# Kernel optimization log

Hardware: AMD Instinct MI355X
Metric: run time of the kernel (lower is better)

Reference implementation:

```python
import jax, jax.numpy as jnp
import numpy as np

B, C, H, W = 2, 256, 56, 56
NH = 8
HD = C // NH
SCALE = HD ** -0.5
BN_EPS = 1e-5


def _linear(x, w, b=None):
    y = jnp.einsum('...i,oi->...o', x, w)
    return y + b if b is not None else y


def _dwconv3(v, w, b):
    # depthwise 3x3, stride 1, pad 1
    y = jax.lax.conv_general_dilated(v, w, (1, 1), 'SAME',
                                     dimension_numbers=('NCHW', 'OIHW', 'NCHW'),
                                     feature_group_count=C)
    return y + b[None, :, None, None]


def _spectral(x, context, qw, kvw, pw, pb, dww, dwb):
    # SpectralCrossAttention, sr_ratio=1 path
    xt = jnp.transpose(x, (0, 2, 3, 1))                    # B,H,W,C
    q = jnp.transpose(_linear(xt, qw), (0, 3, 1, 2))       # B,C,H,W
    ct = jnp.transpose(context, (0, 2, 3, 1))
    kv = _linear(ct, kvw)                                  # B,H,W,2C -> split [2,C]
    k = jnp.transpose(kv[..., :C], (0, 3, 1, 2))
    v = jnp.transpose(kv[..., C:], (0, 3, 1, 2))
    v_local = _dwconv3(v, dww, dwb)
    qf = jnp.fft.rfft2(q, s=(H, W), axes=(-2, -1), norm='ortho')
    kf = jnp.fft.rfft2(k, s=(H, W), axes=(-2, -1), norm='ortho')
    attn_map = jnp.fft.irfft2(qf * kf, s=(H, W), axes=(-2, -1), norm='ortho')
    out = attn_map * v + v_local
    out = _linear(jnp.transpose(out, (0, 2, 3, 1)), pw, pb)
    return jnp.transpose(out, (0, 3, 1, 2))


def _token(x, context, qw, kvw, pw, pb, cw):
    # TokenSpectralResidualCrossAttention, sr_ratio=1 path (de_conv = Identity)
    N = H * W
    xt = jnp.transpose(x.reshape(B, C, N), (0, 2, 1))       # B,N,C
    ct = jnp.transpose(context.reshape(B, C, N), (0, 2, 1))
    q = jnp.transpose(_linear(xt, qw).reshape(B, N, NH, HD), (0, 2, 1, 3))  # B,NH,N,HD
    kv = _linear(ct, kvw).reshape(B, N, 2, NH, HD)
    k = jnp.transpose(kv[:, :, 0], (0, 2, 1, 3))
    v = jnp.transpose(kv[:, :, 1], (0, 2, 1, 3))            # B,NH,N,HD
    attn = jax.nn.softmax(jnp.einsum('bhnd,bhmd->bhnm', q, k) * SCALE, axis=-1)
    x_attn = jnp.transpose(jnp.einsum('bhnm,bhmd->bhnd', attn, v), (0, 2, 1, 3)).reshape(B, N, C)
    v_img = jnp.transpose(v, (0, 1, 3, 2)).reshape(B, C, H, W)
    vf = jnp.fft.rfft2(v_img, s=(H, W), axes=(-2, -1), norm='ortho')
    weight = cw[..., 0] + 1j * cw[..., 1]                   # C,H,W//2+1 complex
    v_res = jnp.fft.irfft2(vf * weight[None], s=(H, W), axes=(-2, -1), norm='ortho')
    v_res = jnp.transpose(v_res.reshape(B, C, N), (0, 2, 1))
    out = _linear(x_attn + v_res, pw, pb)
    return jnp.transpose(out, (0, 2, 1)).reshape(B, C, H, W)


def _fuse(os_, ot, g_w1, g_bn_g, g_bn_b, g_w2, g_b2):
    # spatial_gate: Conv1x1(2C->C, no bias) -> BN(eval: mean0/var1) -> ReLU -> Conv1x1(C->1) -> Sigmoid
    g_in = jnp.concatenate([os_, ot], axis=1)               # B,2C,H,W
    h = jnp.einsum('oc,bchw->bohw', g_w1, g_in)
    h = h / jnp.sqrt(1.0 + BN_EPS) * g_bn_g[None, :, None, None] + g_bn_b[None, :, None, None]
    h = jax.nn.relu(h)
    gate = jax.nn.sigmoid(jnp.einsum('oc,bchw->bohw', g_w2, h) + g_b2[None, :, None, None])
    return gate * os_ + (1.0 - gate) * ot


def setup_inputs():
    key = jax.random.key(0)
    ks = jax.random.split(key, 14)
    p = lambda i, shape, s=0.02: jax.random.normal(ks[i], shape, jnp.float32) * s
    return {
        'x': jax.random.normal(ks[0], (B, C, H, W), jnp.float32),
        'context': jax.random.normal(ks[1], (B, C, H, W), jnp.float32),
        's_q_w': p(2, (C, C)),
        's_kv_w': p(3, (2 * C, C)),
        's_proj_w': p(4, (C, C)),
        's_proj_b': jnp.zeros((C,), jnp.float32),
        's_dw_w': p(5, (C, 1, 3, 3), float(np.sqrt(2.0 / 9.0))),
        's_dw_b': jnp.zeros((C,), jnp.float32),
        't_q_w': p(6, (C, C)),
        't_kv_w': p(7, (2 * C, C)),
        't_proj_w': p(8, (C, C)),
        't_proj_b': jnp.zeros((C,), jnp.float32),
        't_cw': p(9, (C, H, W // 2 + 1, 2)),
        'g_w1': p(10, (C, 2 * C), float(np.sqrt(2.0 / C))),
        'g_bn_g': jnp.ones((C,), jnp.float32),
        'g_bn_b': jnp.zeros((C,), jnp.float32),
        'g_w2': p(11, (1, C), float(np.sqrt(2.0 / C))),
        'g_b2': jnp.zeros((1,), jnp.float32),
    }


def reference(x, context, s_q_w, s_kv_w, s_proj_w, s_proj_b, s_dw_w, s_dw_b,
              t_q_w, t_kv_w, t_proj_w, t_proj_b, t_cw,
              g_w1, g_bn_g, g_bn_b, g_w2, g_b2):
    os_ = _spectral(x, context, s_q_w, s_kv_w, s_proj_w, s_proj_b, s_dw_w, s_dw_b)
    ot = _token(x, context, t_q_w, t_kv_w, t_proj_w, t_proj_b, t_cw)
    return _fuse(os_, ot, g_w1, g_bn_g, g_bn_b, g_w2, g_b2)
```

## Files before the change

### kernel.cpp

```cpp
#include <hip/hip_runtime.h>

namespace {
constexpr int kB = 2;
constexpr int kC = 256;
constexpr int kH = 56;
constexpr int kW = 56;
constexpr int kN = kH * kW;
constexpr int kNH = 8;
constexpr int kHD = 32;
constexpr int kNF = kW / 2 + 1;
constexpr int kSpec = kH * kNF;
constexpr long kCN = (long)kC * kN;
constexpr float kAttScale = 0.17677669529663687f;
constexpr float kLog2e = 1.4426950408889634f;
constexpr float kAng = 6.283185307179586f / 56.0f;
constexpr int TW1F = 0;
constexpr int TW2F = 8192;
constexpr int TW1I = 12288;
constexpr int TW2I = 20480;
constexpr int TWTOT = 24576;
}

typedef __attribute__((ext_vector_type(8))) short short8;
typedef __attribute__((ext_vector_type(4))) float float4v;
// ... 11 lines not shown
}
__device__ __forceinline__ float b2f(unsigned short u) {
    return __uint_as_float((unsigned)u << 16);
}
__device__ __forceinline__ unsigned f2b_pk(float a, float b) {
    unsigned ua = __float_as_uint(a); ua = (ua + 0x7FFFu + ((ua >> 16) & 1u)) >> 16;
    unsigned ub = __float_as_uint(b); ub = (ub + 0x7FFFu + ((ub >> 16) & 1u)) >> 16;
    return ua | (ub << 16);
}
__device__ __forceinline__ unsigned pk_trunc(float a, float b) {
    return (__float_as_uint(a) >> 16) | (__float_as_uint(b) & 0xFFFF0000u);
}
__device__ __forceinline__ uint4 pk8(const float* v) {
    return make_uint4(f2b_pk(v[0], v[1]), f2b_pk(v[2], v[3]),
                      f2b_pk(v[4], v[5]), f2b_pk(v[6], v[7]));
}

__device__ void twiddle_body(int blk, unsigned short* __restrict__ tw)
{
    int idx = blk * 256 + threadIdx.x;
    if (idx >= TWTOT) return;
    float val = 0.f;
    if (idx < TW2F) {
        int r = idx >> 6, c = idx & 63;
        if (c < 56) {
            if (r < 56)       val = cosf(kAng * (float)((r * c) % 56));
            else if (r < 112) val = sinf(kAng * (float)(((r - 56) * c) % 56));
        }
    } else if (idx < TW1I) {
        int t = idx - TW2F; int r = t >> 6, c = t & 63;
        if (c < 56) {
            if (r < 29)                  val = cosf(kAng * (float)((r * c) % 56));
            else if (r >= 32 && r < 61)  val = sinf(kAng * (float)(((r - 32) * c) % 56));
        }
    } else if (idx < TW2I) {
        int t = idx - TW1I; int r = t >> 6, c = t & 63;
        if (c < 56) {
            if (r < 56)                  val = cosf(kAng * (float)((r * c) % 56));
            else if (r >= 64 && r < 120) val = sinf(kAng * (float)(((r - 64) * c) % 56));
        }
    } else {
        int t = idx - TW2I; int x = t >> 6, c = t & 63;
        if (x < 56 && c < 58) {
            int v = c >> 1;
            float wv = ((v == 0) || (v == 28)) ? 1.f : 2.f;
            float a = kAng * (float)((v * x) % 56);
            val = (c & 1) ? (-wv * sinf(a)) : (wv * cosf(a));
        }
    }
    tw[idx] = f2b(val);
}

__device__ void gemm_bias_body(char* smem, const float* __restrict__ Wm,
                               const float* __restrict__ Xb,
                               const float* __restrict__ bias, float* __restrict__ Yb,
                               int o0, int oY, int n0, int CI)
{
    unsigned short (*Wt)[40] = (unsigned short(*)[40])smem;
    unsigned short (*Xt)[40] = (unsigned short(*)[40])(smem + 5120);

    const int tid = threadIdx.x;
    const int wave = tid >> 6, lane = tid & 63;
    const int ln = lane & 15, qd = lane >> 4;
    const int wy = wave >> 1, wx = wave & 1;

    const int ow = tid >> 2, kcw = tid & 3;
    const int nx = tid & 127, kcx = tid >> 7;
    const bool xvalid = (n0 + nx) < kN;

    float4v acc[2][4];
#pragma unroll
    for (int i = 0; i < 2; ++i)
#pragma unroll
        for (int j = 0; j < 4; ++j) acc[i][j] = (float4v){0.f, 0.f, 0.f, 0.f};

    float wpre[8], xpre[16];
    {
        const float* ws = Wm + (long)(o0 + ow) * CI + kcw * 8;
        *(float4*)&wpre[0] = *(const float4*)ws;
        *(float4*)&wpre[4] = *(const float4*)(ws + 4);
#pragma unroll
        for (int j = 0; j < 16; ++j)
            xpre[j] = xvalid ? Xb[(long)(kcx * 16 + j) * kN + n0 + nx] : 0.f;
    }

    for (int k0 = 0; k0 < CI; k0 += 32) {
        *(uint4*)&Wt[ow][kcw * 8]      = pk8(wpre);
        *(uint4*)&Xt[nx][kcx * 16]     = pk8(xpre);
        *(uint4*)&Xt[nx][kcx * 16 + 8] = pk8(xpre + 8);
        __syncthreads();

        if (k0 + 32 < CI) {
            const float* ws = Wm + (long)(o0 + ow) * CI + k0 + 32 + kcw * 8;
            *(float4*)&wpre[0] = *(const float4*)ws;
            *(float4*)&wpre[4] = *(const float4*)(ws + 4);
#pragma unroll
            for (int j = 0; j < 16; ++j)
                xpre[j] = xvalid ? Xb[(long)(k0 + 32 + kcx * 16 + j) * kN + n0 + nx] : 0.f;
        }

        Frag af[2], bf4[4];
#pragma unroll
        for (int mt = 0; mt < 2; ++mt)
            af[mt].u4 = *(const uint4*)&Wt[wy * 32 + mt * 16 + ln][qd * 8];
#pragma unroll
        for (int nt = 0; nt < 4; ++nt)
            bf4[nt].u4 = *(const uint4*)&Xt[wx * 64 + nt * 16 + ln][qd * 8];
#pragma unroll
        for (int mt = 0; mt < 2; ++mt)
#pragma unroll
            for (int nt = 0; nt < 4; ++nt)
                acc[mt][nt] = __builtin_amdgcn_mfma_f32_16x16x32_bf16(
                    af[mt].s, bf4[nt].s, acc[mt][nt], 0, 0, 0);
        __syncthreads();
    }

#pragma unroll
    for (int mt = 0; mt < 2; ++mt) {
        const int obL = o0 + wy * 32 + mt * 16 + qd * 4;
        const int obY = oY + wy * 32 + mt * 16 + qd * 4;
#pragma unroll
        for (int nt = 0; nt < 4; ++nt) {
            const int n = n0 + wx * 64 + nt * 16 + ln;
            if (n < kN) {
#pragma unroll
                for (int r = 0; r < 4; ++r) {
                    float v = acc[mt][nt][r];
                    if (bias) v += bias[obL + r];
                    Yb[(long)(obY + r) * kN + n] = v;
                }
            }
        }
    }
}

__global__ __launch_bounds__(256)
void init_proj_kernel(unsigned short* __restrict__ tw,
                      const float* __restrict__ x, const float* __restrict__ ctx,
                      const float* __restrict__ s_q_w, const float* __restrict__ t_q_w,
                      const float* __restrict__ s_kv_w, const float* __restrict__ t_kv_w,
                      float* __restrict__ sq, float* __restrict__ tq,
                      float* __restrict__ skv, float* __restrict__ tkv)
{
    __shared__ __align__(16) char smem[15360];
    int bi = blockIdx.x;
    if (bi < 96) { twiddle_body(bi, tw); return; }
    bi -= 96;
    if (bi < 400) {
        int b = bi / 200, rem = bi % 200;
        int y = rem / 25, xb = rem % 25;
        int sel = y >= 4;
        int o0 = (sel ? y - 4 : y) * 64;
        gemm_bias_body(smem, sel ? t_q_w : s_q_w, (x + (long)b * kCN), nullptr,
                       (sel ? tq : sq) + (long)b * kCN, o0, o0, xb * 128, kC);
    } else {
        bi -= 400;
        int b = bi / 400, rem = bi % 400;
        int y = rem / 25, xb = rem % 25;
        int sel = y >= 8;
        int o0 = (sel ? y - 8 : y) * 64;
        gemm_bias_body(smem, sel ? t_kv_w : s_kv_w, (ctx + (long)b * kCN), nullptr,
                       (sel ? tkv : skv) + (long)b * 2 * kCN, o0, o0, xb * 128, kC);
    }
}

__device__ void dft_fwd_body(char* smem, int bx,
                             const float* __restrict__ s0, const float* __restrict__ s1,
                             const float* __restrict__ s2, float* __restrict__ d0,
                             float* __restrict__ d1, float* __restrict__ d2,
                             const unsigned short* __restrict__ tw)
{
    const int which = bx >> 9, ch = bx & 511;
    const int b = ch >> 8, c = ch & 255;
    const float* src; long stride; float* spec;
    if (which == 0)      { src = s0; stride = kCN;     spec = d0; }
    else if (which == 1) { src = s1; stride = 2 * kCN; spec = d1; }
    else                 { src = s2; stride = 2 * kCN; spec = d2; }
    const float* img = src + (long)b * stride + (long)c * kN;

    unsigned short (*Gb)[72]    = (unsigned short(*)[72])smem;
    unsigned short (*imgT)[72]  = (unsigned short(*)[72])(smem + 18432);
    unsigned short (*Yb)[116]   = (unsigned short(*)[116])(smem + 18432);

    const int tid = threadIdx.x;
    const int wave = tid >> 6, lane = tid & 63;
    const int ln = lane & 15, qd = lane >> 4;

    for (int i = tid; i < 64 * 72; i += 256) {
        int r = i / 72, cc = i - r * 72;
        if (r >= 56 || cc >= 56) imgT[r][cc] = 0;
    }
    for (int i = tid; i < kN; i += 256) {
        int y = i / 56, x = i - y * 56;
        imgT[x][y] = f2b(img[i]);
    }
    __syncthreads();

    float4v acc1[2][4];
#pragma unroll
    for (int m = 0; m < 2; ++m)
#pragma unroll
        for (int n = 0; n < 4; ++n) acc1[m][n] = (float4v){0.f, 0.f, 0.f, 0.f};
#pragma unroll
    for (int ks = 0; ks < 2; ++ks) {
        Frag a[2], bf[4];
#pragma unroll
        for (int m = 0; m < 2; ++m)
            a[m].u4 = *(const uint4*)(tw + TW1F + ((2 * wave + m) * 16 + ln) * 64 + ks * 32 + qd * 8);
#pragma unroll
        for (int n = 0; n < 4; ++n)
            bf[n].u4 = *(const uint4*)&imgT[n * 16 + ln][ks * 32 + qd * 8];
#pragma unroll
        for (int m = 0; m < 2; ++m)
#pragma unroll
            for (int n = 0; n < 4; ++n)
                acc1[m][n] = __builtin_amdgcn_mfma_f32_16x16x32_bf16(a[m].s, bf[n].s, acc1[m][n], 0, 0, 0);
    }
#pragma unroll
    for (int m = 0; m < 2; ++m)
#pragma unroll
        for (int n = 0; n < 4; ++n)
#pragma unroll
            for (int r = 0; r < 4; ++r)
                Gb[(2 * wave + m) * 16 + qd * 4 + r][n * 16 + ln] = f2b(acc1[m][n][r]);
    __syncthreads();

    float4v acc2[7];
#pragma unroll
    for (int n = 0; n < 7; ++n) acc2[n] = (float4v){0.f, 0.f, 0.f, 0.f};
#pragma unroll
    for (int ks = 0; ks < 2; ++ks) {
        Frag a;
        a.u4 = *(const uint4*)(tw + TW2F + (wave * 16 + ln) * 64 + ks * 32 + qd * 8);
#pragma unroll
        for (int n = 0; n < 7; ++n) {
            Frag bb;
            bb.u4 = *(const uint4*)&Gb[n * 16 + ln][ks * 32 + qd * 8];
            acc2[n] = __builtin_amdgcn_mfma_f32_16x16x32_bf16(a.s, bb.s, acc2[n], 0, 0, 0);
        }
    }
#pragma unroll
    for (int n = 0; n < 7; ++n)
#pragma unroll
        for (int r = 0; r < 4; ++r)
            Yb[wave * 16 + qd * 4 + r][n * 16 + ln] = f2b(acc2[n][r]);
    __syncthreads();

    float2* outp = (float2*)spec + (long)ch * kSpec;
    for (int i = tid; i < kSpec; i += 256) {
        int u = i / kNF, v = i - u * kNF;
        float Qr = b2f(Yb[v][u]) - b2f(Yb[32 + v][56 + u]);
        float Qi = -b2f(Yb[32 + v][u]) - b2f(Yb[v][56 + u]);
        outp[i] = make_float2(Qr, Qi);
    }
}

__device__ void prepack_body(char* smem, int blk, const float* __restrict__ tkv,
                             unsigned short* __restrict__ Kp,
                             unsigned short* __restrict__ Vp)
{
    const int i = blk % 49;
    const int h = (blk / 49) & 7;
    const int b = blk / (49 * 8);
    const float* kb = tkv + (long)b * 2 * kCN + (long)h * kHD * kN;
    const float* vb = kb + kCN;
    const int tid = threadIdx.x;

    float (*Ks)[72] = (float(*)[72])smem;
#pragma unroll
    for (int j = 0; j < 8; ++j) {
        int e = tid + j * 256;
        int d = e >> 6, c = e & 63;
        Ks[d][c] = kb[(long)d * kN + i * 64 + c];
    }
    __syncthreads();
    {
        int tl = tid >> 6, lnn = (tid >> 2) & 15, qdd = tid & 3;
        float v[8];
#pragma unroll
        for (int j = 0; j < 8; ++j) v[j] = Ks[qdd * 8 + j][tl * 16 + lnn];
        unsigned short* dst = Kp + ((long)(b * 8 + h) * 196 + 4 * i + tl) * 512 + lnn * 32 + qdd * 8;
        *(uint4*)dst = pk8(v);
    }
    {
        int g = tid >> 7, dh = (tid >> 6) & 1, lnn = (tid >> 2) & 15, qdd = tid & 3;
        int d = dh * 16 + lnn;
        const float* src = vb + (long)d * kN + i * 64 + g * 32 + qdd * 8;
        float v[8];
        *(float4*)&v[0] = *(const float4*)src;
        *(float4*)&v[4] = *(const float4*)(src + 4);
        unsigned short* dst = Vp + ((long)(b * 8 + h) * 49 + i) * 2048 + ((g * 2 + dh) * 16 + lnn) * 32 + qdd * 8;
        *(uint4*)dst = pk8(v);
    }
}

__global__ __launch_bounds__(256)
void fwd3_prepack_kernel(const float* __restrict__ s0, const float* __restrict__ s1,
                         const float* __restrict__ s2, float* __restrict__ d0,
                         float* __restrict__ d1, float* __restrict__ d2,
                         const unsigned short* __restrict__ tw,
                         const float* __restrict__ tkv,
                         unsigned short* __restrict__ Kp, unsigned short* __restrict__ Vp)
{
    __shared__ __align__(16) char smem[33280];
    if (blockIdx.x < 1536)
        dft_fwd_body(smem, blockIdx.x, s0, s1, s2, d0, d1, d2, tw);
    else
        prepack_body(smem, blockIdx.x - 1536, tkv, Kp, Vp);
}

__device__ void dft_inv_body(char* smem, int bx,
                             const float* __restrict__ fQ, const float* __restrict__ fK,
                             const float* __restrict__ fV, const float* __restrict__ cw,
                             float* __restrict__ dst1, float* __restrict__ dst2,
                             const float* __restrict__ skvp, const float* __restrict__ dww,
                             const float* __restrict__ dwb, const unsigned short* __restrict__ tw)
{
    const int unit = bx >> 9;
    const int ch = bx & 511;
    const int b = ch >> 8, c = ch & 255;
    unsigned short (*Pb)[72]  = (unsigned short(*)[72])smem;
    unsigned short (*Yb)[72]  = (unsigned short(*)[72])(smem + 9216);
    unsigned short (*T2)[72]  = (unsigned short(*)[72])smem;
    float (*svs)[65]          = (float(*)[65])(smem + 9216);

    const int tid = threadIdx.x;
    const int wave = tid >> 6, lane = tid & 63;
    const int ln = lane & 15, qd = lane >> 4;

    const float2* Pin; const float2* Min; float scale; float* dst;
    if (unit == 0) {
        Pin = (const float2*)fQ + (long)ch * kSpec;
        Min = (const float2*)fK + (long)ch * kSpec;
        scale = 1.0f / 175616.0f; dst = dst1;
    } else {
        Pin = (const float2*)fV + (long)ch * kSpec;
        Min = (const float2*)cw + (long)c * kSpec;
        scale = 1.0f / 3136.0f; dst = dst2;
    }

    for (int i = tid; i < 64 * 72; i += 256) {
        int r = i / 72, cc = i - r * 72;
        if (r >= 58 || cc >= 56) Pb[r][cc] = 0;
    }
    for (int i = tid; i < kSpec; i += 256) {
        int u = i / kNF, v = i - u * kNF;
        float2 p = Pin[i];
        float2 m = Min[i];
        float pr = (p.x * m.x - p.y * m.y) * scale;
        float pi = (p.x * m.y + p.y * m.x) * scale;
        Pb[2 * v][u]     = f2b(pr);
        Pb[2 * v + 1][u] = f2b(pi);
    }
    __syncthreads();

    float4v acc1[2][4];
#pragma unroll
    for (int m = 0; m < 2; ++m)
#pragma unroll
        for (int n = 0; n < 4; ++n) acc1[m][n] = (float4v){0.f, 0.f, 0.f, 0.f};
#pragma unroll
// ... 47 lines not shown
        }
#pragma unroll
        for (int j = 0; j < 9; ++j) wreg[j] = dww[c * 9 + j];
        bias = dwb[c];
    }

    float4v acc2[4];
#pragma unroll
    for (int n = 0; n < 4; ++n) acc2[n] = (float4v){0.f, 0.f, 0.f, 0.f};
#pragma unroll
    for (int ks = 0; ks < 2; ++ks) {
        Frag a;
        a.u4 = *(const uint4*)(tw + TW2I + (wave * 16 + ln) * 64 + ks * 32 + qd * 8);
#pragma unroll
        for (int n = 0; n < 4; ++n) {
            Frag bb;
            bb.u4 = *(const uint4*)&T2[n * 16 + ln][ks * 32 + qd * 8];
            acc2[n] = __builtin_amdgcn_mfma_f32_16x16x32_bf16(a.s, bb.s, acc2[n], 0, 0, 0);
        }
    }
    __syncthreads();

    float* outd = dst + (long)ch * kN;
#pragma unroll
    for (int n = 0; n < 4; ++n) {
        int y = n * 16 + ln;
        if (y < 56) {
#pragma unroll
            for (int r = 0; r < 4; ++r) {
                int x = wave * 16 + qd * 4 + r;
                if (x < 56) {
                    int e = y * 56 + x;
                    if (unit == 0) {
                        float s = bias;
                        s = fmaf(wreg[0], svs[y][x],     s);
                        s = fmaf(wreg[1], svs[y][x + 1], s);
                        s = fmaf(wreg[2], svs[y][x + 2], s);
                        s = fmaf(wreg[3], svs[y + 1][x],     s);
                        s = fmaf(wreg[4], svs[y + 1][x + 1], s);
                        s = fmaf(wreg[5], svs[y + 1][x + 2], s);
                        s = fmaf(wreg[6], svs[y + 2][x],     s);
                        s = fmaf(wreg[7], svs[y + 2][x + 1], s);
                        s = fmaf(wreg[8], svs[y + 2][x + 2], s);
                        outd[e] = fmaf(acc2[n][r], svs[y + 1][x + 1], s);
                    } else {
                        outd[e] = acc2[n][r];
                    }
                }
            }
        }
    }
}

__device__ void attn_body(char* smem, int abi,
                          const float* __restrict__ tq,
                          const unsigned short* __restrict__ Kp,
                          const unsigned short* __restrict__ Vp,
                          float* __restrict__ Op, float* __restrict__ lp)
{
    const int xcd = abi & 7;
    const int t = abi >> 3;
    const int gsel = (t >= 100) ? 1 : 0;
    const int r0 = t - gsel * 100;
    const int grpId = (gsel << 3) | xcd;
    const int b = grpId >> 3, h = grpId & 7;
    const int sp = r0 / 25;
    const int q0 = (r0 % 25) * 128;
    const int tid = threadIdx.x;
    const int wave = tid >> 6, lane = tid & 63;
    const int qd = lane >> 4, ln = lane & 15;
    const int i0 = (sp == 0) ? 0 : (12 * sp + 1);
    const int i1 = 12 * sp + 13;

    const float* qb = tq + (long)b * kCN + (long)h * kHD * kN;
    const unsigned short* KpB = Kp + (long)(b * 8 + h) * 196 * 512 + ln * 32 + qd * 8;
    const unsigned short* VpB = Vp + (long)(b * 8 + h) * 49 * 2048 + ln * 32 + qd * 8;

    unsigned short* PsW = (unsigned short*)smem + wave * (32 * 40);

    const float qscale = kAttScale * kLog2e;
    Frag qf[2];
#pragma unroll
    for (int qt = 0; qt < 2; ++qt) {
        int qg = q0 + wave * 32 + qt * 16 + ln;
        bool qv = qg < kN;
#pragma unroll
        for (int j = 0; j < 8; ++j) {
            int d = qd * 8 + j;
            float v = qv ? qb[(long)d * kN + qg] * qscale : 0.f;
            qf[qt].u[j] = f2b(v);
        }
    }

    float4v o[2][2];
#pragma unroll
    for (int qt = 0; qt < 2; ++qt)
#pragma unroll
        for (int dh = 0; dh < 2; ++dh) o[qt][dh] = (float4v){0.f, 0.f, 0.f, 0.f};
    float lsum[2] = {0.f, 0.f};

    unsigned W[4][2][2];
    Frag ka[4];
#pragma unroll
    for (int m = 0; m < 4; ++m)
        ka[m].u4 = *(const uint4*)(KpB + (long)(4 * i0 + m) * 512);

    auto computeW = [&]() {
#pragma unroll
        for (int m = 0; m < 4; ++m) {
            float4v s0 = __builtin_amdgcn_mfma_f32_16x16x32_bf16(
                ka[m].s, qf[0].s, (float4v){0.f, 0.f, 0.f, 0.f}, 0, 0, 0);
            float4v s1 = __builtin_amdgcn_mfma_f32_16x16x32_bf16(
                ka[m].s, qf[1].s, (float4v){0.f, 0.f, 0.f, 0.f}, 0, 0, 0);
            float a0 = __builtin_amdgcn_exp2f(s0[0]);
            float a1 = __builtin_amdgcn_exp2f(s0[1]);
            float a2 = __builtin_amdgcn_exp2f(s0[2]);
            float a3 = __builtin_amdgcn_exp2f(s0[3]);
            lsum[0] += (a0 + a1) + (a2 + a3);
            W[m][0][0] = pk_trunc(a0, a1);
            W[m][0][1] = pk_trunc(a2, a3);
            float b0 = __builtin_amdgcn_exp2f(s1[0]);
            float b1 = __builtin_amdgcn_exp2f(s1[1]);
            float b2 = __builtin_amdgcn_exp2f(s1[2]);
            float b3 = __builtin_amdgcn_exp2f(s1[3]);
            lsum[1] += (b0 + b1) + (b2 + b3);
            W[m][1][0] = pk_trunc(b0, b1);
            W[m][1][1] = pk_trunc(b2, b3);
        }
    };

    computeW();
    if (i0 + 1 < i1) {
#pragma unroll
        for (int m = 0; m < 4; ++m)
            ka[m].u4 = *(const uint4*)(KpB + (long)(4 * (i0 + 1) + m) * 512);
    }

    for (int i = i0; i < i1; ++i) {
        Frag va[2][2];
#pragma unroll
        for (int g = 0; g < 2; ++g)
#pragma unroll
            for (int dh = 0; dh < 2; ++dh)
                va[g][dh].u4 = *(const uint4*)(VpB + (long)i * 2048 + (g * 2 + dh) * 512);

#pragma unroll
        for (int m = 0; m < 4; ++m)
#pragma unroll
            for (int qt = 0; qt < 2; ++qt)
                *(uint2*)&PsW[(qt * 16 + ln) * 40 + m * 16 + qd * 4] =
                    make_uint2(W[m][qt][0], W[m][qt][1]);

        if (i + 1 < i1) {
            computeW();
            if (i + 2 < i1) {
#pragma unroll
                for (int m = 0; m < 4; ++m)
                    ka[m].u4 = *(const uint4*)(KpB + (long)(4 * (i + 2) + m) * 512);
            }
        }

#pragma unroll
        for (int g = 0; g < 2; ++g) {
            Frag pa[2];
#pragma unroll
            for (int qt = 0; qt < 2; ++qt)
                pa[qt].u4 = *(const uint4*)&PsW[(qt * 16 + ln) * 40 + g * 32 + qd * 8];
#pragma unroll
            for (int qt = 0; qt < 2; ++qt)
#pragma unroll
                for (int dh = 0; dh < 2; ++dh)
                    o[qt][dh] = __builtin_amdgcn_mfma_f32_16x16x32_bf16(
                        pa[qt].s, va[g][dh].s, o[qt][dh], 0, 0, 0);
        }
    }

    const long grp = (long)(sp * 16 + b * 8 + h);
#pragma unroll
    for (int qt = 0; qt < 2; ++qt) {
        lsum[qt] += __shfl_xor(lsum[qt], 16, 64);
        lsum[qt] += __shfl_xor(lsum[qt], 32, 64);
        if (qd == 0)
            lp[grp * 3200 + q0 + wave * 32 + qt * 16 + ln] = lsum[qt];
#pragma unroll
        for (int dh = 0; dh < 2; ++dh)
#pragma unroll
            for (int r = 0; r < 4; ++r) {
                int q = q0 + wave * 32 + qt * 16 + qd * 4 + r;
                Op[(grp * 3200 + q) * 32 + dh * 16 + ln] = o[qt][dh][r];
            }
    }
}

__global__ __launch_bounds__(256, 4)
void inv_attn_kernel(const float* __restrict__ fQ, const float* __restrict__ fK,
                     const float* __restrict__ fV, const float* __restrict__ cw,
                     float* __restrict__ dst1, float* __restrict__ dst2,
                     const float* __restrict__ skvp, const float* __restrict__ dww,
                     const float* __restrict__ dwb, const unsigned short* __restrict__ tw,
                     const float* __restrict__ tq,
                     const unsigned short* __restrict__ Kp,
                     const unsigned short* __restrict__ Vp,
                     float* __restrict__ Op, float* __restrict__ lp)
{
    __shared__ __align__(16) char smem[27648];
    const int per = blockIdx.x / 328;
    const int off = blockIdx.x % 328;
    if (off < 128)
        dft_inv_body(smem, per * 128 + off, fQ, fK, fV, cw, dst1, dst2, skvp, dww, dwb, tw);
    else
        attn_body(smem, per * 200 + (off - 128), tq, Kp, Vp, Op, lp);
}

__global__ __launch_bounds__(256)
void attn_combine_kernel(const float* __restrict__ Op, const float* __restrict__ lp,
                         float* __restrict__ xo)
{
    const int qc = blockIdx.x, bh = blockIdx.y;
    const int b = bh >> 3, h = bh & 7;
    const int q0 = qc * 64;
    __shared__ float T[32][65];
    const int tid = threadIdx.x;

    for (int i = tid; i < 64 * 32; i += 256) {
        int ql = i >> 5, d = i & 31;
        float ov = 0.f, l = 0.f;
#pragma unroll
        for (int s = 0; s < 4; ++s) {
            long g = (long)(s * 16 + bh);
            ov += Op[(g * 3200 + q0 + ql) * 32 + d];
            l  += lp[g * 3200 + q0 + ql];
        }
        T[d][ql] = ov / l;
    }
    __syncthreads();
    for (int i = tid; i < 32 * 64; i += 256) {
        int d = i >> 6, ql = i & 63;
        xo[(long)b * kCN + (long)(h * kHD + d) * kN + q0 + ql] += T[d][ql];
    }
}

__global__ __launch_bounds__(256)
void gemm_fused(const float* __restrict__ W0, const float* __restrict__ W1,
                const float* __restrict__ X0, const float* __restrict__ X1,
                const float* __restrict__ b0, const float* __restrict__ b1,
                float* __restrict__ Y0, float* __restrict__ Y1,
                int oHalf, int CI, long xbs, long ybs, int oOffset)
{
    __shared__ __align__(16) char smem[15360];
    const int b  = blockIdx.z;
    const int sel = blockIdx.y >= oHalf;
    const int o0 = (sel ? blockIdx.y - oHalf : blockIdx.y) * 64;
    const int oY = o0 + (sel ? oOffset : 0);
    gemm_bias_body(smem, sel ? W1 : W0, (sel ? X1 : X0) + (long)b * xbs,
                   sel ? b1 : b0, (sel ? Y1 : Y0) + (long)b * ybs,
                   o0, oY, blockIdx.x * 128, CI);
}

__global__ __launch_bounds__(256)
void gemm_bn_kernel(const float* __restrict__ Wm, const float* __restrict__ X,
                    const float* __restrict__ gamma, const float* __restrict__ beta,
                    float* __restrict__ Y, int CI, long xbs, long ybs)
{
    const int b  = blockIdx.z;
    const int o0 = blockIdx.y * 64;
    const int n0 = blockIdx.x * 128;
    const float* Xb = X + (long)b * xbs;
    float* Yb = Y + (long)b * ybs;

    __shared__ __align__(16) unsigned short Wt[64][40];
    __shared__ __align__(16) unsigned short Xt[128][40];

    const int tid = threadIdx.x;
    const int wave = tid >> 6, lane = tid & 63;
    const int ln = lane & 15, qd = lane >> 4;
    const int wy = wave >> 1, wx = wave & 1;

    const int ow = tid >> 2, kcw = tid & 3;
    const int nx = tid & 127, kcx = tid >> 7;
    const bool xvalid = (n0 + nx) < kN;

    float4v acc[2][4];
#pragma unroll
    for (int i = 0; i < 2; ++i)
#pragma unroll
        for (int j = 0; j < 4; ++j) acc[i][j] = (float4v){0.f, 0.f, 0.f, 0.f};

    float wpre[8], xpre[16];
    {
        const float* ws = Wm + (long)(o0 + ow) * CI + kcw * 8;
        *(float4*)&wpre[0] = *(const float4*)ws;
        *(float4*)&wpre[4] = *(const float4*)(ws + 4);
#pragma unroll
        for (int j = 0; j < 16; ++j)
            xpre[j] = xvalid ? Xb[(long)(kcx * 16 + j) * kN + n0 + nx] : 0.f;
    }

    for (int k0 = 0; k0 < CI; k0 += 32) {
        *(uint4*)&Wt[ow][kcw * 8]      = pk8(wpre);
        *(uint4*)&Xt[nx][kcx * 16]     = pk8(xpre);
        *(uint4*)&Xt[nx][kcx * 16 + 8] = pk8(xpre + 8);
        __syncthreads();

        if (k0 + 32 < CI) {
            const float* ws = Wm + (long)(o0 + ow) * CI + k0 + 32 + kcw * 8;
            *(float4*)&wpre[0] = *(const float4*)ws;
            *(float4*)&wpre[4] = *(const float4*)(ws + 4);
// ... 66 lines not shown
    float* op = out + (long)b * kCN + n0 + lane;
    for (int c = g; c < kC; c += 4) {
        float os = osp[(long)c * kN];
        float ot = otp[(long)c * kN];
        op[(long)c * kN] = gt * os + (1.f - gt) * ot;
    }
}

extern "C" void kernel_launch(void* const* d_in, const int* in_sizes, int n_in,
                              void* d_out, int out_size, void* d_ws, size_t ws_size,
                              hipStream_t stream)
{
    const float* x      = (const float*)d_in[0];
    const float* ctx    = (const float*)d_in[1];
    const float* s_q_w  = (const float*)d_in[2];
    const float* s_kv_w = (const float*)d_in[3];
    const float* s_p_w  = (const float*)d_in[4];
    const float* s_p_b  = (const float*)d_in[5];
    const float* s_dw_w = (const float*)d_in[6];
    const float* s_dw_b = (const float*)d_in[7];
    const float* t_q_w  = (const float*)d_in[8];
    const float* t_kv_w = (const float*)d_in[9];
    const float* t_p_w  = (const float*)d_in[10];
    const float* t_p_b  = (const float*)d_in[11];
    const float* t_cw   = (const float*)d_in[12];
    const float* g_w1   = (const float*)d_in[13];
    const float* g_bn_g = (const float*)d_in[14];
    const float* g_bn_b = (const float*)d_in[15];
    const float* g_w2   = (const float*)d_in[16];
    const float* g_b2   = (const float*)d_in[17];
    float* out = (float*)d_out;

    float* ws = (float*)d_ws;
    const long SPEC2 = (long)kB * kC * kSpec * 2;
    float* sq   = ws;
    float* skv  = sq   + kB * kCN;
    float* tq   = skv  + kB * 2 * kCN;
    float* tkv  = tq   + kB * kCN;
    float* vloc = tkv  + kB * 2 * kCN;
    float* fQ   = vloc + kB * kCN;
    float* fK   = fQ   + SPEC2;
    float* fV   = fK   + SPEC2;
    float* gcat = fV   + SPEC2;
    float* gate = gcat + kB * 2 * kCN;
    unsigned short* tw = (unsigned short*)(gate + kB * kN);
    unsigned short* Kp = tw + TWTOT;
    unsigned short* Vp = Kp + (long)16 * 196 * 512;
    float* Opart = (float*)(Vp + (long)16 * 49 * 2048);
    float* lpart = Opart + (long)64 * 3200 * 32;

    dim3 blk(256, 1, 1);

    init_proj_kernel<<<dim3(1296), blk, 0, stream>>>(
        tw, x, ctx, s_q_w, t_q_w, s_kv_w, t_kv_w, sq, tq, skv, tkv);

    fwd3_prepack_kernel<<<dim3(3 * kB * kC + kB * kNH * 49), blk, 0, stream>>>(
        sq, skv, tkv + kCN, fQ, fK, fV, tw, tkv, Kp, Vp);

    inv_attn_kernel<<<dim3(2624), blk, 0, stream>>>(
        fQ, fK, fV, t_cw, vloc, sq, skv, s_dw_w, s_dw_b, tw,
        tq, Kp, Vp, Opart, lpart);

    attn_combine_kernel<<<dim3(49, 16), blk, 0, stream>>>(Opart, lpart, sq);

    gemm_fused<<<dim3(25, 8, kB), blk, 0, stream>>>(
        s_p_w, t_p_w, vloc, sq, s_p_b, t_p_b, gcat, gcat, 4, kC, kCN, 2 * kCN, 256);

    gemm_bn_kernel<<<dim3(25, 4, kB), blk, 0, stream>>>(g_w1, gcat, g_bn_g, g_bn_b, tkv, 2 * kC, 2 * kCN, kCN);

    gateblend_kernel<<<dim3(49, kB), blk, 0, stream>>>(tkv, g_w2, g_b2, gcat, out);
}
```

Measured before the change: 266.1 us.

## Fuse K/V prepack into projection GEMM and reschedule attention alongside forward DFT

Measured after the change: 301.2 us. +13.2%, slower.

```diff
diff --git a/kernel.cpp b/kernel.cpp
--- a/kernel.cpp
+++ b/kernel.cpp
@@ -87,7 +87,7 @@
 }
 
 __device__ void gemm_bias_body(char* smem, const float* __restrict__ Wm,
-                               const float* __restrict__ Xb,
+                               const float* __restrict__ Xb, const float* __restrict__ Xadd,
                                const float* __restrict__ bias, float* __restrict__ Yb,
                                int o0, int oY, int n0, int CI)
 {
@@ -115,8 +115,10 @@
         *(float4*)&wpre[0] = *(const float4*)ws;
         *(float4*)&wpre[4] = *(const float4*)(ws + 4);
 #pragma unroll
-        for (int j = 0; j < 16; ++j)
-            xpre[j] = xvalid ? Xb[(long)(kcx * 16 + j) * kN + n0 + nx] : 0.f;
+        for (int j = 0; j < 16; ++j) {
+            long e = (long)(kcx * 16 + j) * kN + n0 + nx;
+            xpre[j] = xvalid ? (Xadd ? Xb[e] + Xadd[e] : Xb[e]) : 0.f;
+        }
     }
 
     for (int k0 = 0; k0 < CI; k0 += 32) {
@@ -130,8 +132,10 @@
             *(float4*)&wpre[0] = *(const float4*)ws;
             *(float4*)&wpre[4] = *(const float4*)(ws + 4);
 #pragma unroll
-            for (int j = 0; j < 16; ++j)
-                xpre[j] = xvalid ? Xb[(long)(k0 + 32 + kcx * 16 + j) * kN + n0 + nx] : 0.f;
+            for (int j = 0; j < 16; ++j) {
+                long e = (long)(k0 + 32 + kcx * 16 + j) * kN + n0 + nx;
+                xpre[j] = xvalid ? (Xadd ? Xb[e] + Xadd[e] : Xb[e]) : 0.f;
+            }
         }
 
         Frag af[2], bf4[4];
@@ -169,15 +173,151 @@
     }
 }
 
+__device__ void gemm_kv_token_body(char* smem, const float* __restrict__ Wm,
+                                   const float* __restrict__ Xb, float* __restrict__ Yb,
+                                   int b, int o0, int n0,
+                                   unsigned short* __restrict__ Kp,
+                                   unsigned short* __restrict__ Vp)
+{
+    unsigned short (*Wt)[40] = (unsigned short(*)[40])smem;
+    unsigned short (*Xt)[40] = (unsigned short(*)[40])(smem + 5120);
+
+    const int tid = threadIdx.x;
+    const int wave = tid >> 6, lane = tid & 63;
+    const int ln = lane & 15, qd = lane >> 4;
+    const int wy = wave >> 1, wx = wave & 1;
+
+    const int ow = tid >> 2, kcw = tid & 3;
+    const int nx = tid & 127, kcx = tid >> 7;
+    const bool xvalid = (n0 + nx) < kN;
+
+    float4v acc[2][4];
+#pragma unroll
+    for (int i = 0; i < 2; ++i)
+#pragma unroll
+        for (int j = 0; j < 4; ++j) acc[i][j] = (float4v){0.f, 0.f, 0.f, 0.f};
+
+    float wpre[8], xpre[16];
+    {
+        const float* ws = Wm + (long)(o0 + ow) * kC + kcw * 8;
+        *(float4*)&wpre[0] = *(const float4*)ws;
+        *(float4*)&wpre[4] = *(const float4*)(ws + 4);
+#pragma unroll
+        for (int j = 0; j < 16; ++j)
+            xpre[j] = xvalid ? Xb[(long)(kcx * 16 + j) * kN + n0 + nx] : 0.f;
+    }
+
+    for (int k0 = 0; k0 < kC; k0 += 32) {
+        *(uint4*)&Wt[ow][kcw * 8]      = pk8(wpre);
+        *(uint4*)&Xt[nx][kcx * 16]     = pk8(xpre);
+        *(uint4*)&Xt[nx][kcx * 16 + 8] = pk8(xpre + 8);
+        __syncthreads();
+
+        if (k0 + 32 < kC) {
+            const float* ws = Wm + (long)(o0 + ow) * kC + k0 + 32 + kcw * 8;
+            *(float4*)&wpre[0] = *(const float4*)ws;
+            *(float4*)&wpre[4] = *(const float4*)(ws + 4);
+#pragma unroll
+            for (int j = 0; j < 16; ++j)
+                xpre[j] = xvalid ? Xb[(long)(k0 + 32 + kcx * 16 + j) * kN + n0 + nx] : 0.f;
+        }
+
+        Frag af[2], bf4[4];
+#pragma unroll
+        for (int mt = 0; mt < 2; ++mt)
+            af[mt].u4 = *(const uint4*)&Wt[wy * 32 + mt * 16 + ln][qd * 8];
+#pragma unroll
+        for (int nt = 0; nt < 4; ++nt)
+            bf4[nt].u4 = *(const uint4*)&Xt[wx * 64 + nt * 16 + ln][qd * 8];
+#pragma unroll
+        for (int mt = 0; mt < 2; ++mt)
+#pragma unroll
+            for (int nt = 0; nt < 4; ++nt)
+                acc[mt][nt] = __builtin_amdgcn_mfma_f32_16x16x32_bf16(
+                    af[mt].s, bf4[nt].s, acc[mt][nt], 0, 0, 0);
+        __syncthreads();
+    }
+
+    const bool isK = (o0 < 256);
+
+    if (!isK) {
+#pragma unroll
+        for (int mt = 0; mt < 2; ++mt) {
+            const int ob = o0 + wy * 32 + mt * 16 + qd * 4;
+#pragma unroll
+            for (int nt = 0; nt < 4; ++nt) {
+                const int n = n0 + wx * 64 + nt * 16 + ln;
+                if (n < kN) {
+#pragma unroll
+                    for (int r = 0; r < 4; ++r)
+                        Yb[(long)(ob + r) * kN + n] = acc[mt][nt][r];
+                }
+            }
+        }
+    }
+
+    unsigned short (*T)[72] = (unsigned short(*)[72])smem;
+#pragma unroll
+    for (int mt = 0; mt < 2; ++mt)
+#pragma unroll
+        for (int nt = 0; nt < 4; ++nt) {
+            int nloc = wx * 64 + nt * 16 + ln;
+            int oloc = wy * 32 + mt * 16 + qd * 4;
+            *(uint2*)&T[nloc][oloc] =
+                make_uint2(f2b_pk(acc[mt][nt][0], acc[mt][nt][1]),
+                           f2b_pk(acc[mt][nt][2], acc[mt][nt][3]));
+        }
+    __syncthreads();
+
+    const int h0 = (isK ? o0 : o0 - 256) >> 5;
+    if (isK) {
+#pragma unroll
+        for (int j = 0; j < 4; ++j) {
+            int idx = tid + j * 256;
+            int hh = idx >> 9, t = (idx >> 6) & 7, lnn = (idx >> 2) & 15, qdd = idx & 3;
+            int key = n0 + t * 16 + lnn;
+            if (key < kN) {
+                uint4 v = *(const uint4*)&T[t * 16 + lnn][hh * 32 + qdd * 8];
+                unsigned short* dst = Kp + ((long)(b * 8 + h0 + hh) * 196 + (key >> 4)) * 512
+                                      + (key & 15) * 32 + qdd * 8;
+                *(uint4*)dst = v;
+            }
+        }
+    } else {
+#pragma unroll
+        for (int j = 0; j < 4; ++j) {
+            int idx = tid + j * 256;
+            int hh = idx >> 9, kt2 = (idx >> 8) & 1, g = (idx >> 7) & 1;
+            int dh = (idx >> 6) & 1, dl = (idx >> 2) & 15, k8 = idx & 3;
+            int keyb = n0 + kt2 * 64 + g * 32 + k8 * 8;
+            if (keyb < kN) {
+                int oloc = hh * 32 + dh * 16 + dl;
+                int nb = kt2 * 64 + g * 32 + k8 * 8;
+                unsigned short vv[8];
+#pragma unroll
+                for (int kk = 0; kk < 8; ++kk) vv[kk] = T[nb + kk][oloc];
+                uint4 v = make_uint4((unsigned)vv[0] | ((unsigned)vv[1] << 16),
+                                     (unsigned)vv[2] | ((unsigned)vv[3] << 16),
+                                     (unsigned)vv[4] | ((unsigned)vv[5] << 16),
+                                     (unsigned)vv[6] | ((unsigned)vv[7] << 16));
+                unsigned short* dst = Vp + ((long)(b * 8 + h0 + hh) * 49 + (n0 >> 6) + kt2) * 2048
+                                      + (g * 2 + dh) * 512 + dl * 32 + k8 * 8;
+                *(uint4*)dst = v;
+            }
+        }
+    }
+}
+
 __global__ __launch_bounds__(256)
 void init_proj_kernel(unsigned short* __restrict__ tw,
                       const float* __restrict__ x, const float* __restrict__ ctx,
                       const float* __restrict__ s_q_w, const float* __restrict__ t_q_w,
                       const float* __restrict__ s_kv_w, const float* __restrict__ t_kv_w,
                       float* __restrict__ sq, float* __restrict__ tq,
-                      float* __restrict__ skv, float* __restrict__ tkv)
-{
-    __shared__ __align__(16) char smem[15360];
+                      float* __restrict__ skv, float* __restrict__ tkv,
+                      unsigned short* __restrict__ Kp, unsigned short* __restrict__ Vp)
+{
+    __shared__ __align__(16) char smem[18432];
     int bi = blockIdx.x;
     if (bi < 96) { twiddle_body(bi, tw); return; }
     bi -= 96;
@@ -186,16 +326,20 @@
         int y = rem / 25, xb = rem % 25;
         int sel = y >= 4;
         int o0 = (sel ? y - 4 : y) * 64;
-        gemm_bias_body(smem, sel ? t_q_w : s_q_w, (x + (long)b * kCN), nullptr,
+        gemm_bias_body(smem, sel ? t_q_w : s_q_w, x + (long)b * kCN, nullptr, nullptr,
                        (sel ? tq : sq) + (long)b * kCN, o0, o0, xb * 128, kC);
+    } else if (bi < 800) {
+        bi -= 400;
+        int b = bi / 200, rem = bi % 200;
+        int y = rem / 25, xb = rem % 25;
+        gemm_bias_body(smem, s_kv_w, ctx + (long)b * kCN, nullptr, nullptr,
+                       skv + (long)b * 2 * kCN, y * 64, y * 64, xb * 128, kC);
     } else {
-        bi -= 400;
-        int b = bi / 400, rem = bi % 400;
+        bi -= 800;
+        int b = bi / 200, rem = bi % 200;
         int y = rem / 25, xb = rem % 25;
-        int sel = y >= 8;
-        int o0 = (sel ? y - 8 : y) * 64;
-        gemm_bias_body(smem, sel ? t_kv_w : s_kv_w, (ctx + (long)b * kCN), nullptr,
-                       (sel ? tkv : skv) + (long)b * 2 * kCN, o0, o0, xb * 128, kC);
+        gemm_kv_token_body(smem, t_kv_w, ctx + (long)b * kCN,
+                           tkv + (long)b * 2 * kCN, b, y * 64, xb * 128, Kp, Vp);
     }
 }
 
@@ -290,58 +434,163 @@
     }
 }
 
-__device__ void prepack_body(char* smem, int blk, const float* __restrict__ tkv,
-                             unsigned short* __restrict__ Kp,
-                             unsigned short* __restrict__ Vp)
-{
-    const int i = blk % 49;
-    const int h = (blk / 49) & 7;
-    const int b = blk / (49 * 8);
-    const float* kb = tkv + (long)b * 2 * kCN + (long)h * kHD * kN;
-    const float* vb = kb + kCN;
+__device__ void attn_body(char* smem, int abi,
+                          const float* __restrict__ tq,
+                          const unsigned short* __restrict__ Kp,
+                          const unsigned short* __restrict__ Vp,
+                          float* __restrict__ Op, float* __restrict__ lp)
+{
+    const int xcd = abi & 7;
+    const int t = abi >> 3;
+    const int gsel = (t >= 100) ? 1 : 0;
+    const int r0 = t - gsel * 100;
+    const int grpId = (gsel << 3) | xcd;
+    const int b = grpId >> 3, h = grpId & 7;
+    const int sp = r0 / 25;
+    const int q0 = (r0 % 25) * 128;
     const int tid = threadIdx.x;
-
-    float (*Ks)[72] = (float(*)[72])smem;
-#pragma unroll
-    for (int j = 0; j < 8; ++j) {
-        int e = tid + j * 256;
-        int d = e >> 6, c = e & 63;
-        Ks[d][c] = kb[(long)d * kN + i * 64 + c];
-    }
-    __syncthreads();
-    {
-        int tl = tid >> 6, lnn = (tid >> 2) & 15, qdd = tid & 3;
-        float v[8];
-#pragma unroll
-        for (int j = 0; j < 8; ++j) v[j] = Ks[qdd * 8 + j][tl * 16 + lnn];
-        unsigned short* dst = Kp + ((long)(b * 8 + h) * 196 + 4 * i + tl) * 512 + lnn * 32 + qdd * 8;
-        *(uint4*)dst = pk8(v);
-    }
-    {
-        int g = tid >> 7, dh = (tid >> 6) & 1, lnn = (tid >> 2) & 15, qdd = tid & 3;
-        int d = dh * 16 + lnn;
-        const float* src = vb + (long)d * kN + i * 64 + g * 32 + qdd * 8;
-        float v[8];
-        *(float4*)&v[0] = *(const float4*)src;
-        *(float4*)&v[4] = *(const float4*)(src + 4);
-        unsigned short* dst = Vp + ((long)(b * 8 + h) * 49 + i) * 2048 + ((g * 2 + dh) * 16 + lnn) * 32 + qdd * 8;
-        *(uint4*)dst = pk8(v);
-    }
-}
-
-__global__ __launch_bounds__(256)
-void fwd3_prepack_kernel(const float* __restrict__ s0, const float* __restrict__ s1,
-                         const float* __restrict__ s2, float* __restrict__ d0,
-                         float* __restrict__ d1, float* __restrict__ d2,
-                         const unsigned short* __restrict__ tw,
-                         const float* __restrict__ tkv,
-                         unsigned short* __restrict__ Kp, unsigned short* __restrict__ Vp)
+    const int wave = tid >> 6, lane = tid & 63;
+    const int qd = lane >> 4, ln = lane & 15;
+    const int i0 = (sp == 0) ? 0 : (12 * sp + 1);
+    const int i1 = 12 * sp + 13;
+
+    const float* qb = tq + (long)b * kCN + (long)h * kHD * kN;
+    const unsigned short* KpB = Kp + (long)(b * 8 + h) * 196 * 512 + ln * 32 + qd * 8;
+    const unsigned short* VpB = Vp + (long)(b * 8 + h) * 49 * 2048 + ln * 32 + qd * 8;
+
+    unsigned short* PsW = (unsigned short*)smem + wave * (32 * 40);
+
+    const float qscale = kAttScale * kLog2e;
+    Frag qf[2];
+#pragma unroll
+    for (int qt = 0; qt < 2; ++qt) {
+        int qg = q0 + wave * 32 + qt * 16 + ln;
+        bool qv = qg < kN;
+#pragma unroll
+        for (int j = 0; j < 8; ++j) {
+            int d = qd * 8 + j;
+            float v = qv ? qb[(long)d * kN + qg] * qscale : 0.f;
+            qf[qt].u[j] = f2b(v);
+        }
+    }
+
+    float4v o[2][2];
+#pragma unroll
+    for (int qt = 0; qt < 2; ++qt)
+#pragma unroll
+        for (int dh = 0; dh < 2; ++dh) o[qt][dh] = (float4v){0.f, 0.f, 0.f, 0.f};
+    float lsum[2] = {0.f, 0.f};
+
+    unsigned W[4][2][2];
+    Frag ka[4];
+#pragma unroll
+    for (int m = 0; m < 4; ++m)
+        ka[m].u4 = *(const uint4*)(KpB + (long)(4 * i0 + m) * 512);
+
+    auto computeW = [&]() {
+#pragma unroll
+        for (int m = 0; m < 4; ++m) {
+            float4v s0 = __builtin_amdgcn_mfma_f32_16x16x32_bf16(
+                ka[m].s, qf[0].s, (float4v){0.f, 0.f, 0.f, 0.f}, 0, 0, 0);
+            float4v s1 = __builtin_amdgcn_mfma_f32_16x16x32_bf16(
+                ka[m].s, qf[1].s, (float4v){0.f, 0.f, 0.f, 0.f}, 0, 0, 0);
+            float a0 = __builtin_amdgcn_exp2f(s0[0]);
+            float a1 = __builtin_amdgcn_exp2f(s0[1]);
+            float a2 = __builtin_amdgcn_exp2f(s0[2]);
+            float a3 = __builtin_amdgcn_exp2f(s0[3]);
+            lsum[0] += (a0 + a1) + (a2 + a3);
+            W[m][0][0] = pk_trunc(a0, a1);
+            W[m][0][1] = pk_trunc(a2, a3);
+            float b0 = __builtin_amdgcn_exp2f(s1[0]);
+            float b1 = __builtin_amdgcn_exp2f(s1[1]);
+            float b2 = __builtin_amdgcn_exp2f(s1[2]);
+            float b3 = __builtin_amdgcn_exp2f(s1[3]);
+            lsum[1] += (b0 + b1) + (b2 + b3);
+            W[m][1][0] = pk_trunc(b0, b1);
+            W[m][1][1] = pk_trunc(b2, b3);
+        }
+    };
+
+    computeW();
+    if (i0 + 1 < i1) {
+#pragma unroll
+        for (int m = 0; m < 4; ++m)
+            ka[m].u4 = *(const uint4*)(KpB + (long)(4 * (i0 + 1) + m) * 512);
+    }
+
+    for (int i = i0; i < i1; ++i) {
+        Frag va[2][2];
+#pragma unroll
+        for (int g = 0; g < 2; ++g)
+#pragma unroll
+            for (int dh = 0; dh < 2; ++dh)
+                va[g][dh].u4 = *(const uint4*)(VpB + (long)i * 2048 + (g * 2 + dh) * 512);
+
+#pragma unroll
+        for (int m = 0; m < 4; ++m)
+#pragma unroll
+            for (int qt = 0; qt < 2; ++qt)
+                *(uint2*)&PsW[(qt * 16 + ln) * 40 + m * 16 + qd * 4] =
+                    make_uint2(W[m][qt][0], W[m][qt][1]);
+
+        if (i + 1 < i1) {
+            computeW();
+            if (i + 2 < i1) {
+#pragma unroll
+                for (int m = 0; m < 4; ++m)
+                    ka[m].u4 = *(const uint4*)(KpB + (long)(4 * (i + 2) + m) * 512);
+            }
+        }
+
+#pragma unroll
+        for (int g = 0; g < 2; ++g) {
+            Frag pa[2];
+#pragma unroll
+            for (int qt = 0; qt < 2; ++qt)
+                pa[qt].u4 = *(const uint4*)&PsW[(qt * 16 + ln) * 40 + g * 32 + qd * 8];
+#pragma unroll
+            for (int qt = 0; qt < 2; ++qt)
+#pragma unroll
+                for (int dh = 0; dh < 2; ++dh)
+                    o[qt][dh] = __builtin_amdgcn_mfma_f32_16x16x32_bf16(
+                        pa[qt].s, va[g][dh].s, o[qt][dh], 0, 0, 0);
+        }
+    }
+
+    const long grp = (long)(sp * 16 + b * 8 + h);
+#pragma unroll
+    for (int qt = 0; qt < 2; ++qt) {
+        lsum[qt] += __shfl_xor(lsum[qt], 16, 64);
+        lsum[qt] += __shfl_xor(lsum[qt], 32, 64);
+        if (qd == 0)
+            lp[grp * 3200 + q0 + wave * 32 + qt * 16 + ln] = lsum[qt];
+#pragma unroll
+        for (int dh = 0; dh < 2; ++dh)
+#pragma unroll
+            for (int r = 0; r < 4; ++r) {
+                int q = q0 + wave * 32 + qt * 16 + qd * 4 + r;
+                Op[(grp * 3200 + q) * 32 + dh * 16 + ln] = o[qt][dh][r];
+            }
+    }
+}
+
+__global__ __launch_bounds__(256, 4)
+void fwd3_attn_kernel(const float* __restrict__ s0, const float* __restrict__ s1,
+                      const float* __restrict__ s2, float* __restrict__ d0,
+                      float* __restrict__ d1, float* __restrict__ d2,
+                      const unsigned short* __restrict__ tw,
+                      const float* __restrict__ tq,
+                      const unsigned short* __restrict__ Kp,
+                      const unsigned short* __restrict__ Vp,
+                      float* __restrict__ Op, float* __restrict__ lp)
 {
     __shared__ __align__(16) char smem[33280];
-    if (blockIdx.x < 1536)
-        dft_fwd_body(smem, blockIdx.x, s0, s1, s2, d0, d1, d2, tw);
+    const int per = blockIdx.x / 392;
+    const int off = blockIdx.x % 392;
+    if (off < 192)
+        dft_fwd_body(smem, per * 192 + off, s0, s1, s2, d0, d1, d2, tw);
     else
-        prepack_body(smem, blockIdx.x - 1536, tkv, Kp, Vp);
+        attn_body(smem, per * 200 + (off - 192), tq, Kp, Vp, Op, lp);
 }
 
 __device__ void dft_inv_body(char* smem, int bx,
@@ -495,174 +744,14 @@
     }
 }
 
-__device__ void attn_body(char* smem, int abi,
-                          const float* __restrict__ tq,
-                          const unsigned short* __restrict__ Kp,
-                          const unsigned short* __restrict__ Vp,
-                          float* __restrict__ Op, float* __restrict__ lp)
-{
-    const int xcd = abi & 7;
-    const int t = abi >> 3;
-    const int gsel = (t >= 100) ? 1 : 0;
-    const int r0 = t - gsel * 100;
-    const int grpId = (gsel << 3) | xcd;
-    const int b = grpId >> 3, h = grpId & 7;
-    const int sp = r0 / 25;
-    const int q0 = (r0 % 25) * 128;
-    const int tid = threadIdx.x;
-    const int wave = tid >> 6, lane = tid & 63;
-    const int qd = lane >> 4, ln = lane & 15;
-    const int i0 = (sp == 0) ? 0 : (12 * sp + 1);
-    const int i1 = 12 * sp + 13;
-
-    const float* qb = tq + (long)b * kCN + (long)h * kHD * kN;
-    const unsigned short* KpB = Kp + (long)(b * 8 + h) * 196 * 512 + ln * 32 + qd * 8;
-    const unsigned short* VpB = Vp + (long)(b * 8 + h) * 49 * 2048 + ln * 32 + qd * 8;
-
-    unsigned short* PsW = (unsigned short*)smem + wave * (32 * 40);
-
-    const float qscale = kAttScale * kLog2e;
-    Frag qf[2];
-#pragma unroll
-    for (int qt = 0; qt < 2; ++qt) {
-        int qg = q0 + wave * 32 + qt * 16 + ln;
-        bool qv = qg < kN;
-#pragma unroll
-        for (int j = 0; j < 8; ++j) {
-            int d = qd * 8 + j;
-            float v = qv ? qb[(long)d * kN + qg] * qscale : 0.f;
-            qf[qt].u[j] = f2b(v);
-        }
-    }
-
-    float4v o[2][2];
-#pragma unroll
-    for (int qt = 0; qt < 2; ++qt)
-#pragma unroll
-        for (int dh = 0; dh < 2; ++dh) o[qt][dh] = (float4v){0.f, 0.f, 0.f, 0.f};
-    float lsum[2] = {0.f, 0.f};
-
-    unsigned W[4][2][2];
-    Frag ka[4];
-#pragma unroll
-    for (int m = 0; m < 4; ++m)
-        ka[m].u4 = *(const uint4*)(KpB + (long)(4 * i0 + m) * 512);
-
-    auto computeW = [&]() {
-#pragma unroll
-        for (int m = 0; m < 4; ++m) {
-            float4v s0 = __builtin_amdgcn_mfma_f32_16x16x32_bf16(
-                ka[m].s, qf[0].s, (float4v){0.f, 0.f, 0.f, 0.f}, 0, 0, 0);
-            float4v s1 = __builtin_amdgcn_mfma_f32_16x16x32_bf16(
-                ka[m].s, qf[1].s, (float4v){0.f, 0.f, 0.f, 0.f}, 0, 0, 0);
-            float a0 = __builtin_amdgcn_exp2f(s0[0]);
-            float a1 = __builtin_amdgcn_exp2f(s0[1]);
-            float a2 = __builtin_amdgcn_exp2f(s0[2]);
-            float a3 = __builtin_amdgcn_exp2f(s0[3]);
-            lsum[0] += (a0 + a1) + (a2 + a3);
-            W[m][0][0] = pk_trunc(a0, a1);
-            W[m][0][1] = pk_trunc(a2, a3);
-            float b0 = __builtin_amdgcn_exp2f(s1[0]);
-            float b1 = __builtin_amdgcn_exp2f(s1[1]);
-            float b2 = __builtin_amdgcn_exp2f(s1[2]);
-            float b3 = __builtin_amdgcn_exp2f(s1[3]);
-            lsum[1] += (b0 + b1) + (b2 + b3);
-            W[m][1][0] = pk_trunc(b0, b1);
-            W[m][1][1] = pk_trunc(b2, b3);
-        }
-    };
-
-    computeW();
-    if (i0 + 1 < i1) {
-#pragma unroll
-        for (int m = 0; m < 4; ++m)
-            ka[m].u4 = *(const uint4*)(KpB + (long)(4 * (i0 + 1) + m) * 512);
-    }
-
-    for (int i = i0; i < i1; ++i) {
-        Frag va[2][2];
-#pragma unroll
-        for (int g = 0; g < 2; ++g)
-#pragma unroll
-            for (int dh = 0; dh < 2; ++dh)
-                va[g][dh].u4 = *(const uint4*)(VpB + (long)i * 2048 + (g * 2 + dh) * 512);
-
-#pragma unroll
-        for (int m = 0; m < 4; ++m)
-#pragma unroll
-            for (int qt = 0; qt < 2; ++qt)
-                *(uint2*)&PsW[(qt * 16 + ln) * 40 + m * 16 + qd * 4] =
-                    make_uint2(W[m][qt][0], W[m][qt][1]);
-
-        if (i + 1 < i1) {
-            computeW();
-            if (i + 2 < i1) {
-#pragma unroll
-                for (int m = 0; m < 4; ++m)
-                    ka[m].u4 = *(const uint4*)(KpB + (long)(4 * (i + 2) + m) * 512);
-            }
-        }
-
-#pragma unroll
-        for (int g = 0; g < 2; ++g) {
-            Frag pa[2];
-#pragma unroll
-            for (int qt = 0; qt < 2; ++qt)
-                pa[qt].u4 = *(const uint4*)&PsW[(qt * 16 + ln) * 40 + g * 32 + qd * 8];
-#pragma unroll
-            for (int qt = 0; qt < 2; ++qt)
-#pragma unroll
-                for (int dh = 0; dh < 2; ++dh)
-                    o[qt][dh] = __builtin_amdgcn_mfma_f32_16x16x32_bf16(
-                        pa[qt].s, va[g][dh].s, o[qt][dh], 0, 0, 0);
-        }
-    }
-
-    const long grp = (long)(sp * 16 + b * 8 + h);
-#pragma unroll
-    for (int qt = 0; qt < 2; ++qt) {
-        lsum[qt] += __shfl_xor(lsum[qt], 16, 64);
-        lsum[qt] += __shfl_xor(lsum[qt], 32, 64);
-        if (qd == 0)
-            lp[grp * 3200 + q0 + wave * 32 + qt * 16 + ln] = lsum[qt];
-#pragma unroll
-        for (int dh = 0; dh < 2; ++dh)
-#pragma unroll
-            for (int r = 0; r < 4; ++r) {
-                int q = q0 + wave * 32 + qt * 16 + qd * 4 + r;
-                Op[(grp * 3200 + q) * 32 + dh * 16 + ln] = o[qt][dh][r];
-            }
-    }
-}
-
-__global__ __launch_bounds__(256, 4)
-void inv_attn_kernel(const float* __restrict__ fQ, const float* __restrict__ fK,
-                     const float* __restrict__ fV, const float* __restrict__ cw,
-                     float* __restrict__ dst1, float* __restrict__ dst2,
-                     const float* __restrict__ skvp, const float* __restrict__ dww,
-                     const float* __restrict__ dwb, const unsigned short* __restrict__ tw,
-                     const float* __restrict__ tq,
-                     const unsigned short* __restrict__ Kp,
-                     const unsigned short* __restrict__ Vp,
-                     float* __restrict__ Op, float* __restrict__ lp)
-{
-    __shared__ __align__(16) char smem[27648];
-    const int per = blockIdx.x / 328;
-    const int off = blockIdx.x % 328;
-    if (off < 128)
-        dft_inv_body(smem, per * 128 + off, fQ, fK, fV, cw, dst1, dst2, skvp, dww, dwb, tw);
-    else
-        attn_body(smem, per * 200 + (off - 128), tq, Kp, Vp, Op, lp);
-}
-
-__global__ __launch_bounds__(256)
-void attn_combine_kernel(const float* __restrict__ Op, const float* __restrict__ lp,
-                         float* __restrict__ xo)
-{
-    const int qc = blockIdx.x, bh = blockIdx.y;
+__device__ void combine_body(char* smem, int cb,
+                             const float* __restrict__ Op, const float* __restrict__ lp,
+                             float* __restrict__ xat)
+{
+    const int qc = cb % 49, bh = cb / 49;
     const int b = bh >> 3, h = bh & 7;
     const int q0 = qc * 64;
-    __shared__ float T[32][65];
+    float (*T)[65] = (float(*)[65])smem;
     const int tid = threadIdx.x;
 
     for (int i = tid; i < 64 * 32; i += 256) {
@@ -679,13 +768,32 @@
     __syncthreads();
     for (int i = tid; i < 32 * 64; i += 256) {
         int d = i >> 6, ql = i & 63;
-        xo[(long)b * kCN + (long)(h * kHD + d) * kN + q0 + ql] += T[d][ql];
-    }
+        xat[(long)b * kCN + (long)(h * kHD + d) * kN + q0 + ql] = T[d][ql];
+    }
+}
+
+__global__ __launch_bounds__(256)
+void inv_combine_kernel(const float* __restrict__ fQ, const float* __restrict__ fK,
+                        const float* __restrict__ fV, const float* __restrict__ cw,
+                        float* __restrict__ dst1, float* __restrict__ dst2,
+                        const float* __restrict__ skvp, const float* __restrict__ dww,
+                        const float* __restrict__ dwb, const unsigned short* __restrict__ tw,
+                        const float* __restrict__ Op, const float* __restrict__ lp,
+                        float* __restrict__ xat)
+{
+    __shared__ __align__(16) char smem[27648];
+    const int per = blockIdx.x / 113;
+    const int off = blockIdx.x % 113;
+    if (off < 64)
+        dft_inv_body(smem, per * 64 + off, fQ, fK, fV, cw, dst1, dst2, skvp, dww, dwb, tw);
+    else
+        combine_body(smem, per * 49 + (off - 64), Op, lp, xat);
 }
 
 __global__ __launch_bounds__(256)
 void gemm_fused(const float* __restrict__ W0, const float* __restrict__ W1,
                 const float* __restrict__ X0, const float* __restrict__ X1,
+                const float* __restrict__ X1add,
                 const float* __restrict__ b0, const float* __restrict__ b1,
                 float* __restrict__ Y0, float* __restrict__ Y1,
                 int oHalf, int CI, long xbs, long ybs, int oOffset)
@@ -696,6 +804,7 @@
     const int o0 = (sel ? blockIdx.y - oHalf : blockIdx.y) * 64;
     const int oY = o0 + (sel ? oOffset : 0);
     gemm_bias_body(smem, sel ? W1 : W0, (sel ? X1 : X0) + (long)b * xbs,
+                   sel ? (X1add + (long)b * xbs) : nullptr,
                    sel ? b1 : b0, (sel ? Y1 : Y0) + (long)b * ybs,
                    o0, oY, blockIdx.x * 128, CI);
 }
@@ -868,19 +977,16 @@
     dim3 blk(256, 1, 1);
 
     init_proj_kernel<<<dim3(1296), blk, 0, stream>>>(
-        tw, x, ctx, s_q_w, t_q_w, s_kv_w, t_kv_w, sq, tq, skv, tkv);
-
-    fwd3_prepack_kernel<<<dim3(3 * kB * kC + kB * kNH * 49), blk, 0, stream>>>(
-        sq, skv, tkv + kCN, fQ, fK, fV, tw, tkv, Kp, Vp);
-
-    inv_attn_kernel<<<dim3(2624), blk, 0, stream>>>(
-        fQ, fK, fV, t_cw, vloc, sq, skv, s_dw_w, s_dw_b, tw,
-        tq, Kp, Vp, Opart, lpart);
-
-    attn_combine_kernel<<<dim3(49, 16), blk, 0, stream>>>(Opart, lpart, sq);
+        tw, x, ctx, s_q_w, t_q_w, s_kv_w, t_kv_w, sq, tq, skv, tkv, Kp, Vp);
+
+    fwd3_attn_kernel<<<dim3(3136), blk, 0, stream>>>(
+        sq, skv, tkv + kCN, fQ, fK, fV, tw, tq, Kp, Vp, Opart, lpart);
+
+    inv_combine_kernel<<<dim3(1808), blk, 0, stream>>>(
+        fQ, fK, fV, t_cw, vloc, sq, skv, s_dw_w, s_dw_b, tw, Opart, lpart, tq);
 
     gemm_fused<<<dim3(25, 8, kB), blk, 0, stream>>>(
-        s_p_w, t_p_w, vloc, sq, s_p_b, t_p_b, gcat, gcat, 4, kC, kCN, 2 * kCN, 256);
+        s_p_w, t_p_w, vloc, sq, tq, s_p_b, t_p_b, gcat, gcat, 4, kC, kCN, 2 * kCN, 256);
 
     gemm_bn_kernel<<<dim3(25, 4, kB), blk, 0, stream>>>(g_w1, gcat, g_bn_g, g_bn_b, tkv, 2 * kC, 2 * kCN, kCN);
 
```
